# Optimization experiments

Hardware: AMD Instinct MI355X
Metric: run time of the kernel (lower is better)

## Reference

```python
import jax, jax.numpy as jnp
import numpy as np

D = 1024
H = 16
DH = D // H  # 64

def setup_inputs() -> dict:
    key = jax.random.key(0)
    ks = jax.random.split(key, 9)
    B, S = 2, 2048
    s = 1.0 / np.sqrt(D)
    return {
        "embed": jax.random.normal(ks[0], (B, S, D), dtype=jnp.float32),
        "Wq": jax.random.normal(ks[1], (D, D), dtype=jnp.float32) * s,
        "Wk": jax.random.normal(ks[2], (D, D), dtype=jnp.float32) * s,
        "Wv": jax.random.normal(ks[3], (D, D), dtype=jnp.float32) * s,
        "bv": jax.random.normal(ks[4], (D,), dtype=jnp.float32) * 0.01,
        "W1": jax.random.normal(ks[5], (2 * D, D), dtype=jnp.float32) * s,
        "b1": jax.random.normal(ks[6], (2 * D,), dtype=jnp.float32) * 0.01,
        "W2": jax.random.normal(ks[7], (D, 2 * D), dtype=jnp.float32) * (1.0 / np.sqrt(2 * D)),
        "b2": jax.random.normal(ks[8], (D,), dtype=jnp.float32) * 0.01,
    }

def reference(embed, Wq, Wk, Wv, bv, W1, b1, W2, b2):
    B, S, _ = embed.shape
    # torch nn.Linear: y = x @ W.T (+ b)
    Q = embed @ Wq.T                      # [B,S,D]
    K = embed @ Wk.T                      # [B,S,D]
    V = embed @ Wv.T + bv                 # [B,S,D]
    # split heads: the per-head python loop in the original is a vmap over H
    Qh = Q.reshape(B, S, H, DH)
    Kh = K.reshape(B, S, H, DH)
    Vh = V.reshape(B, S, H, DH)
    scores = jnp.einsum('bqhd,bkhd->bhqk', Qh, Kh) / np.sqrt(DH)
    attn = jax.nn.softmax(scores, axis=-1)          # [B,H,S,S]
    out = jnp.einsum('bhqk,bkhd->bqhd', attn, Vh).reshape(B, S, D)
    # FFN (use_ffn)
    out = jax.nn.relu(out @ W1.T + b1) @ W2.T + b2
    # residual (use_residue)
    return out + embed
```

## Files before the change

### kernel.cpp

```cpp
#include <hip/hip_runtime.h>
#include <hip/hip_bf16.h>

typedef unsigned short u16;
typedef unsigned int u32;
typedef __attribute__((ext_vector_type(8))) short short8;
typedef __attribute__((ext_vector_type(4))) float f32x4;
typedef __attribute__((ext_vector_type(4))) u16 u16x4;
typedef __attribute__((ext_vector_type(4))) u32 u32x4;

__device__ __forceinline__ u16 f2bf(float f) {
  unsigned u = __builtin_bit_cast(unsigned, f);
  u = (u + 0x7FFFu + ((u >> 16) & 1u)) >> 16;
  return (u16)u;
}

__device__ __forceinline__ u32 cvt_pk_bf16(float lo, float hi) {
  u32 r;
  asm("v_cvt_pk_bf16_f32 %0, %1, %2" : "=v"(r) : "v"(lo), "v"(hi));
  return r;
}

__device__ __forceinline__ void gload16(const void* g, void* l) {
  __builtin_amdgcn_global_load_lds(
      (const __attribute__((address_space(1))) void*)g,
      (__attribute__((address_space(3))) void*)l, 16, 0, 0);
}

__global__ __launch_bounds__(256) void cvt_all(
    const float* __restrict__ e, const float* __restrict__ wq,
    const float* __restrict__ wk, const float* __restrict__ wv,
    const float* __restrict__ w1, const float* __restrict__ w2,
    u16* __restrict__ ebf, u16* __restrict__ wqkv,
    u16* __restrict__ w1b, u16* __restrict__ w2b)
{
  int i = blockIdx.x * 256 + threadIdx.x;
  const float* src;
  u16* dst;
  if (i < 1048576)       { src = e;  dst = ebf; }
  else if (i < 1310720)  { src = wq; dst = wqkv;           i -= 1048576; }
  else if (i < 1572864)  { src = wk; dst = wqkv + 1048576; i -= 1310720; }
  else if (i < 1835008)  { src = wv; dst = wqkv + 2097152; i -= 1572864; }
  else if (i < 2359296)  { src = w1; dst = w1b;            i -= 1835008; }
  else                   { src = w2; dst = w2b;            i -= 2359296; }
  const float4 v = reinterpret_cast<const float4*>(src)[i];
  u16x4 o = { f2bf(v.x), f2bf(v.y), f2bf(v.z), f2bf(v.w) };
  *reinterpret_cast<u16x4*>(dst + (size_t)i * 4) = o;
}

template<int MODE, int BM>
__global__ __launch_bounds__(256, 3) void gemm_bt(
    const u16* __restrict__ A, const u16* __restrict__ W,
    const float* __restrict__ bias, const float* __restrict__ resid,
    void* __restrict__ out0, void* __restrict__ out1, void* __restrict__ out2,
    int M, int N, int K)
{
  constexpr int II = BM / 32;
  __shared__ __align__(16) u16 At[BM * 64];
  __shared__ __align__(16) u16 Bt[128 * 64];
  const int tid = threadIdx.x, lane = tid & 63, wid = tid >> 6;
  const int g = lane >> 4, c = lane & 15;
  const int wr = (wid >> 1) * (BM / 2), wc = (wid & 1) * 64;
  const int m0 = blockIdx.y * BM, n0 = blockIdx.x * 128;
  const int lrow = lane >> 3;
  const int lch = (lane & 7) ^ lrow;
  const int rsw = c & 7;

  f32x4 acc[II][4];
  #pragma unroll
  for (int i = 0; i < II; i++)
    #pragma unroll
    for (int j = 0; j < 4; j++)
      acc[i][j] = (f32x4){0.f, 0.f, 0.f, 0.f};

  const u16* Ab = A + (size_t)m0 * K;
  const u16* Wb = W + (size_t)n0 * K;

  for (int k0 = 0; k0 < K; k0 += 64) {
    __syncthreads();
    #pragma unroll
    for (int i = 0; i < II; i++) {
      const int r0 = (wid * II + i) * 8;
      gload16(Ab + (size_t)(r0 + lrow) * K + k0 + lch * 8, &At[r0 * 64]);
    }
    #pragma unroll
    for (int i = 0; i < 4; i++) {
      const int r0 = (wid * 4 + i) * 8;
      gload16(Wb + (size_t)(r0 + lrow) * K + k0 + lch * 8, &Bt[r0 * 64]);
    }
    __syncthreads();
    #pragma unroll
    for (int kh = 0; kh < 2; kh++) {
      short8 af[II], bw[4];
      #pragma unroll
      for (int i = 0; i < II; i++)
        af[i] = *reinterpret_cast<const short8*>(
            &At[(wr + i * 16 + c) * 64 + (((g + 4 * kh) ^ rsw) * 8)]);
      #pragma unroll
      for (int j = 0; j < 4; j++)
        bw[j] = *reinterpret_cast<const short8*>(
            &Bt[(wc + j * 16 + c) * 64 + (((g + 4 * kh) ^ rsw) * 8)]);
      #pragma unroll
      for (int i = 0; i < II; i++)
        #pragma unroll
        for (int j = 0; j < 4; j++)
          acc[i][j] = __builtin_amdgcn_mfma_f32_16x16x32_bf16(af[i], bw[j], acc[i][j], 0, 0, 0);
    }
  }

  #pragma unroll
  for (int i = 0; i < II; i++) {
    #pragma unroll
    for (int j = 0; j < 4; j++) {
      const int n = n0 + wc + j * 16 + c;
      const int mb = m0 + wr + i * 16 + g * 4;
      if (MODE == 1) {
        const int seg = n >> 10, nn = n & 1023;
        const int h = nn >> 6, d = nn & 63;
        const int bb = mb >> 11, s = mb & 2047;
        if (seg == 2) {
          const float bval = bias[nn];
          u16x4 o;
          #pragma unroll
          for (int r = 0; r < 4; r++) o[r] = f2bf(acc[i][j][r] + bval);
          const int s32 = s & 31;
          const int t2 = (s & ~31) + ((s32 >> 2) & 3) * 8 + ((s32 >> 4) & 1) * 4;
          *reinterpret_cast<u16x4*>(reinterpret_cast<u16*>(out2) +
              ((size_t)((bb << 4) + h) * 64 + d) * 2048 + t2) = o;
        } else {
          u16* dst = reinterpret_cast<u16*>(seg ? out1 : out0);
          const float sc = seg ? 1.0f : 0.18033688f;
          #pragma unroll
          for (int r = 0; r < 4; r++)
            dst[((size_t)((bb << 4) + h) * 2048 + s + r) * 64 + d] = f2bf(acc[i][j][r] * sc);
        }
      } else if (MODE == 3) {
        const float bval = bias[n];
        #pragma unroll
        for (int r = 0; r < 4; r++) {
          float v = fmaxf(acc[i][j][r] + bval, 0.f);
          reinterpret_cast<u16*>(out0)[(size_t)(mb + r) * N + n] = f2bf(v);
        }
      } else {
        const float bval = bias[n];
        #pragma unroll
        for (int r = 0; r < 4; r++) {
          const int m = mb + r;
          reinterpret_cast<float*>(out0)[(size_t)m * N + n] =
              acc[i][j][r] + bval + resid[(size_t)m * N + n];
        }
      }
    }
  }
}

__global__ __launch_bounds__(256, 4) void attn_kernel(
    const u16* __restrict__ Qh, const u16* __restrict__ Kh,
    const u16* __restrict__ Vt, u16* __restrict__ apart,
    float* __restrict__ lpart)
{
  __shared__ __align__(16) u16 Kt[2][64 * 64];
  __shared__ __align__(16) u16 Vl[2][64 * 64];

  const int tid = threadIdx.x;
  const int lane = tid & 63, wid = tid >> 6;
  const int g = lane >> 4, c = lane & 15;

  const int v = (blockIdx.x & 7) * 128 + (blockIdx.x >> 3);
  const int half = v >> 9, rem = v & 511;
  const int bh = rem >> 4, xq = rem & 15;
  const int q0 = xq * 128 + wid * 32;
  const int tbase = half * 1024;

  const int lrow = lane >> 3;
  const int lch = (lane & 7) ^ lrow;
  const int rsw = c & 7;

  short8 bq[2][2];
  #pragma unroll
  for (int qt = 0; qt < 2; qt++) {
    const u16* qrow = Qh + ((size_t)bh * 2048 + q0 + qt * 16 + c) * 64;
    bq[qt][0] = *reinterpret_cast<const short8*>(qrow + g * 8);
    bq[qt][1] = *reinterpret_cast<const short8*>(qrow + 32 + g * 8);
  }

  f32x4 acc[2][4];
  #pragma unroll
  for (int qt = 0; qt < 2; qt++)
    #pragma unroll
    for (int dt = 0; dt < 4; dt++)
      acc[qt][dt] = (f32x4){0.f, 0.f, 0.f, 0.f};
  f32x4 accl[2] = {(f32x4){0.f, 0.f, 0.f, 0.f}, (f32x4){0.f, 0.f, 0.f, 0.f}};
  const short8 ones = {0x3F80, 0x3F80, 0x3F80, 0x3F80, 0x3F80, 0x3F80, 0x3F80, 0x3F80};

  const u16* Kb = Kh + (size_t)bh * 2048 * 64;
  const u16* Vb = Vt + (size_t)bh * 64 * 2048;

  auto stage = [&](int buf, int t0) {
    #pragma unroll
    for (int i = 0; i < 2; i++) {
      const int r0 = (wid * 2 + i) * 8;
      gload16(Kb + (size_t)(t0 + r0 + lrow) * 64 + lch * 8, &Kt[buf][r0 * 64]);
    }
    #pragma unroll
    for (int i = 0; i < 2; i++) {
      const int r0 = (wid * 2 + i) * 8;
      gload16(Vb + (size_t)(r0 + lrow) * 2048 + t0 + lch * 8, &Vl[buf][r0 * 64]);
    }
  };

  stage(0, tbase);

  int cur = 0;
  for (int t0 = tbase; t0 < tbase + 1024; t0 += 64, cur ^= 1) {
    __syncthreads();
    if (t0 + 64 < tbase + 1024) stage(cur ^ 1, t0 + 64);

    #pragma unroll
    for (int cp = 0; cp < 2; cp++) {
      f32x4 sv[2][2];
      __builtin_amdgcn_s_setprio(1);
      #pragma unroll
      for (int h = 0; h < 2; h++) {
        const u16* kr = &Kt[cur][(cp * 32 + h * 16 + c) * 64];
        short8 ka  = *reinterpret_cast<const short8*>(kr + ((g ^ rsw) * 8));
        short8 ka2 = *reinterpret_cast<const short8*>(kr + (((g + 4) ^ rsw) * 8));
        #pragma unroll
        for (int qt = 0; qt < 2; qt++) {
          f32x4 z = (f32x4){0.f, 0.f, 0.f, 0.f};
          z = __builtin_amdgcn_mfma_f32_16x16x32_bf16(ka, bq[qt][0], z, 0, 0, 0);
          z = __builtin_amdgcn_mfma_f32_16x16x32_bf16(ka2, bq[qt][1], z, 0, 0, 0);
          sv[qt][h] = z;
        }
      }
      __builtin_amdgcn_s_setprio(0);

      short8 pk[2];
      #pragma unroll
      for (int qt = 0; qt < 2; qt++) {
        float p[8];
        #pragma unroll
        for (int i = 0; i < 8; i++)
          p[i] = __builtin_amdgcn_exp2f(sv[qt][i >> 2][i & 3]);
        u32x4 w;
        #pragma unroll
        for (int k = 0; k < 4; k++)
          w[k] = cvt_pk_bf16(p[2 * k], p[2 * k + 1]);
        pk[qt] = __builtin_bit_cast(short8, w);
      }

      __builtin_amdgcn_s_setprio(1);
      #pragma unroll
      for (int dt = 0; dt < 4; dt++) {
        const short8 vf = *reinterpret_cast<const short8*>(
            &Vl[cur][(dt * 16 + c) * 64 + (((cp * 4 + g) ^ rsw) * 8)]);
        acc[0][dt] = __builtin_amdgcn_mfma_f32_16x16x32_bf16(pk[0], vf, acc[0][dt], 0, 0, 0);
        acc[1][dt] = __builtin_amdgcn_mfma_f32_16x16x32_bf16(pk[1], vf, acc[1][dt], 0, 0, 0);
      }
      accl[0] = __builtin_amdgcn_mfma_f32_16x16x32_bf16(pk[0], ones, accl[0], 0, 0, 0);
      accl[1] = __builtin_amdgcn_mfma_f32_16x16x32_bf16(pk[1], ones, accl[1], 0, 0, 0);
      __builtin_amdgcn_s_setprio(0);
    }
  }

  u16* ob = apart + ((size_t)(half * 32 + bh) * 2048) * 64;
  #pragma unroll
  for (int qt = 0; qt < 2; qt++) {
    #pragma unroll
    for (int dt = 0; dt < 4; dt++)
      #pragma unroll
      for (int r = 0; r < 4; r++) {
        const size_t q = q0 + qt * 16 + g * 4 + r;
        ob[q * 64 + dt * 16 + c] = f2bf(acc[qt][dt][r]);
      }
    if (c == 0) {
      #pragma unroll
      for (int r = 0; r < 4; r++)
        lpart[(size_t)(half * 32 + bh) * 2048 + q0 + qt * 16 + g * 4 + r] = accl[qt][r];
    }
  }
}

__global__ __launch_bounds__(256) void attn_combine(
    const u16* __restrict__ apart, const float* __restrict__ lpart,
    u16* __restrict__ ao)
{
  const int idx = blockIdx.x * 256 + threadIdx.x;
  const int d4 = idx & 15;
  const int q = (idx >> 4) & 2047;
  const int bh = idx >> 15;
  const size_t p0 = ((size_t)bh * 2048 + q) * 64 + d4 * 4;
  const size_t p1 = ((size_t)(32 + bh) * 2048 + q) * 64 + d4 * 4;
  u16x4 a0 = *reinterpret_cast<const u16x4*>(apart + p0);
  u16x4 a1 = *reinterpret_cast<const u16x4*>(apart + p1);
  const float l = lpart[(size_t)bh * 2048 + q] + lpart[(size_t)(32 + bh) * 2048 + q];
  const float inv = 1.0f / l;
  u16x4 o;
  #pragma unroll
  for (int i = 0; i < 4; i++) {
    const float f0 = __builtin_bit_cast(float, (u32)a0[i] << 16);
    const float f1 = __builtin_bit_cast(float, (u32)a1[i] << 16);
    o[i] = f2bf((f0 + f1) * inv);
  }
  *reinterpret_cast<u16x4*>(
      ao + ((size_t)(bh >> 4) * 2048 + q) * 1024 + (bh & 15) * 64 + d4 * 4) = o;
}

extern "C" void kernel_launch(void* const* d_in, const int* in_sizes, int n_in,
                              void* d_out, int out_size, void* d_ws, size_t ws_size,
                              hipStream_t stream) {
  const float* embed = (const float*)d_in[0];
  const float* Wq = (const float*)d_in[1];
  const float* Wk = (const float*)d_in[2];
  const float* Wv = (const float*)d_in[3];
  const float* bv = (const float*)d_in[4];
  const float* W1 = (const float*)d_in[5];
  const float* b1 = (const float*)d_in[6];
  const float* W2 = (const float*)d_in[7];
  const float* b2 = (const float*)d_in[8];

  char* ws = (char*)d_ws;
  u16* ebf  = (u16*)ws;  ws += (size_t)4096 * 1024 * 2;
  u16* wqkv = (u16*)ws;  ws += (size_t)3072 * 1024 * 2;
  u16* w1b  = (u16*)ws;  ws += (size_t)2048 * 1024 * 2;
  u16* w2b  = (u16*)ws;  ws += (size_t)1024 * 2048 * 2;
  u16* Qh   = (u16*)ws;  ws += (size_t)4096 * 1024 * 2;
  u16* Kh   = (u16*)ws;  ws += (size_t)4096 * 1024 * 2;
  u16* Vt   = (u16*)ws;  ws += (size_t)4096 * 1024 * 2;
  u16* ao   = (u16*)ws;  ws += (size_t)4096 * 1024 * 2;
  u16* h1   = (u16*)ws;  ws += (size_t)4096 * 2048 * 2;

  u16* apart = h1;
  float* lpart = (float*)ebf;

  dim3 blk(256);
  cvt_all<<<dim3(11264), blk, 0, stream>>>(embed, Wq, Wk, Wv, W1, W2,
                                           ebf, wqkv, w1b, w2b);
  gemm_bt<1, 128><<<dim3(24, 32), blk, 0, stream>>>(
      ebf, wqkv, bv, nullptr, Qh, Kh, Vt, 4096, 3072, 1024);
  attn_kernel<<<dim3(1024), blk, 0, stream>>>(Qh, Kh, Vt, apart, lpart);
  attn_combine<<<dim3(4096), blk, 0, stream>>>(apart, lpart, ao);
  gemm_bt<3, 128><<<dim3(16, 32), blk, 0, stream>>>(
      ao, w1b, b1, nullptr, h1, nullptr, nullptr, 4096, 2048, 1024);
  gemm_bt<4, 64><<<dim3(8, 64), blk, 0, stream>>>(
      h1, w2b, b2, embed, d_out, nullptr, nullptr, 4096, 1024, 2048);
}
```

Baseline: 145.3 us.

## Fuse split-KV attention combine into attention kernel via atomic last-arriver

Removes the separate attn_combine launch. Each attention block writes its partial output and row sums, then bumps a per-tile atomic counter. The second block to arrive for a query tile merges its in-register accumulator with the peer's partial from memory and writes the normalized head output directly. This cuts one kernel launch and half of the partial-buffer reads. The cost is threadfences, an atomic, and a counter reset added to the conversion kernel, while the first-arriving blocks still write partials.

```diff
diff --git a/kernel.cpp b/kernel.cpp
--- a/kernel.cpp
+++ b/kernel.cpp
@@ -31,8 +31,12 @@
     const float* __restrict__ wk, const float* __restrict__ wv,
     const float* __restrict__ w1, const float* __restrict__ w2,
     u16* __restrict__ ebf, u16* __restrict__ wqkv,
-    u16* __restrict__ w1b, u16* __restrict__ w2b)
+    u16* __restrict__ w1b, u16* __restrict__ w2b, u32* __restrict__ cnt)
 {
+  if (blockIdx.x == 0) {
+    cnt[threadIdx.x] = 0;
+    cnt[256 + threadIdx.x] = 0;
+  }
   int i = blockIdx.x * 256 + threadIdx.x;
   const float* src;
   u16* dst;
@@ -156,10 +160,11 @@
 __global__ __launch_bounds__(256, 4) void attn_kernel(
     const u16* __restrict__ Qh, const u16* __restrict__ Kh,
     const u16* __restrict__ Vt, u16* __restrict__ apart,
-    float* __restrict__ lpart)
+    float* __restrict__ lpart, u32* __restrict__ cnt, u16* __restrict__ ao)
 {
   __shared__ __align__(16) u16 Kt[2][64 * 64];
   __shared__ __align__(16) u16 Vl[2][64 * 64];
+  __shared__ u32 role;
 
   const int tid = threadIdx.x;
   const int lane = tid & 63, wid = tid >> 6;
@@ -278,31 +283,33 @@
         lpart[(size_t)(half * 32 + bh) * 2048 + q0 + qt * 16 + g * 4 + r] = accl[qt][r];
     }
   }
-}
-
-__global__ __launch_bounds__(256) void attn_combine(
-    const u16* __restrict__ apart, const float* __restrict__ lpart,
-    u16* __restrict__ ao)
-{
-  const int idx = blockIdx.x * 256 + threadIdx.x;
-  const int d4 = idx & 15;
-  const int q = (idx >> 4) & 2047;
-  const int bh = idx >> 15;
-  const size_t p0 = ((size_t)bh * 2048 + q) * 64 + d4 * 4;
-  const size_t p1 = ((size_t)(32 + bh) * 2048 + q) * 64 + d4 * 4;
-  u16x4 a0 = *reinterpret_cast<const u16x4*>(apart + p0);
-  u16x4 a1 = *reinterpret_cast<const u16x4*>(apart + p1);
-  const float l = lpart[(size_t)bh * 2048 + q] + lpart[(size_t)(32 + bh) * 2048 + q];
-  const float inv = 1.0f / l;
-  u16x4 o;
-  #pragma unroll
-  for (int i = 0; i < 4; i++) {
-    const float f0 = __builtin_bit_cast(float, (u32)a0[i] << 16);
-    const float f1 = __builtin_bit_cast(float, (u32)a1[i] << 16);
-    o[i] = f2bf((f0 + f1) * inv);
-  }
-  *reinterpret_cast<u16x4*>(
-      ao + ((size_t)(bh >> 4) * 2048 + q) * 1024 + (bh & 15) * 64 + d4 * 4) = o;
+
+  __threadfence();
+  __syncthreads();
+  if (tid == 0) role = atomicAdd(&cnt[rem], 1u);
+  __syncthreads();
+  if (role == 0) return;
+
+  __threadfence();
+  const u16* pb = apart + ((size_t)((1 - half) * 32 + bh) * 2048) * 64;
+  const float* pl = lpart + (size_t)((1 - half) * 32 + bh) * 2048;
+  u16* aob = ao + (size_t)(bh >> 4) * 2048 * 1024 + (bh & 15) * 64;
+  #pragma unroll
+  for (int qt = 0; qt < 2; qt++) {
+    float lq[4];
+    #pragma unroll
+    for (int r = 0; r < 4; r++)
+      lq[r] = 1.0f / (accl[qt][r] + pl[q0 + qt * 16 + g * 4 + r]);
+    #pragma unroll
+    for (int dt = 0; dt < 4; dt++)
+      #pragma unroll
+      for (int r = 0; r < 4; r++) {
+        const size_t q = q0 + qt * 16 + g * 4 + r;
+        const float peer = __builtin_bit_cast(
+            float, (u32)pb[q * 64 + dt * 16 + c] << 16);
+        aob[q * 1024 + dt * 16 + c] = f2bf((acc[qt][dt][r] + peer) * lq[r]);
+      }
+  }
 }
 
 extern "C" void kernel_launch(void* const* d_in, const int* in_sizes, int n_in,
@@ -328,17 +335,17 @@
   u16* Vt   = (u16*)ws;  ws += (size_t)4096 * 1024 * 2;
   u16* ao   = (u16*)ws;  ws += (size_t)4096 * 1024 * 2;
   u16* h1   = (u16*)ws;  ws += (size_t)4096 * 2048 * 2;
+  u32* cnt  = (u32*)ws;  ws += 512 * 4;
 
   u16* apart = h1;
   float* lpart = (float*)ebf;
 
   dim3 blk(256);
   cvt_all<<<dim3(11264), blk, 0, stream>>>(embed, Wq, Wk, Wv, W1, W2,
-                                           ebf, wqkv, w1b, w2b);
+                                           ebf, wqkv, w1b, w2b, cnt);
   gemm_bt<1, 128><<<dim3(24, 32), blk, 0, stream>>>(
       ebf, wqkv, bv, nullptr, Qh, Kh, Vt, 4096, 3072, 1024);
-  attn_kernel<<<dim3(1024), blk, 0, stream>>>(Qh, Kh, Vt, apart, lpart);
-  attn_combine<<<dim3(4096), blk, 0, stream>>>(apart, lpart, ao);
+  attn_kernel<<<dim3(1024), blk, 0, stream>>>(Qh, Kh, Vt, apart, lpart, cnt, ao);
   gemm_bt<3, 128><<<dim3(16, 32), blk, 0, stream>>>(
       ao, w1b, b1, nullptr, h1, nullptr, nullptr, 4096, 2048, 1024);
   gemm_bt<4, 64><<<dim3(8, 64), blk, 0, stream>>>(
```

Result: slower. 379.3 us (+161.0%).
